# Optimization experiments

Hardware: AMD Instinct MI355X
Metric: run time of the kernel (lower is better)

## Reference

```python
import jax, jax.numpy as jnp
from jax import lax
import numpy as np

B, D, L = 32, 64, 4096
E = 8          # num_experts
K = 2          # top-k
OC = 32        # out_channels


def setup_inputs() -> dict:
    key = jax.random.key(0)
    ks = jax.random.split(key, 6)
    x = jax.random.normal(ks[0], (B, D, L), dtype=jnp.float32)
    # gating weight [D*5, E] (torch init is zeros; use small random for a meaningful reference)
    w_gate = jax.random.normal(ks[1], (D * 5, E), dtype=jnp.float32) * 0.02
    # Conv1d(D -> OC, kernel 3)
    conv1_w = jax.random.normal(ks[2], (OC, D, 3), dtype=jnp.float32) * (1.0 / np.sqrt(D * 3))
    conv1_b = jax.random.normal(ks[3], (OC,), dtype=jnp.float32) * 0.01
    # Conv1d(OC -> OC*E, kernel 1)
    conv2_w = jax.random.normal(ks[4], (OC * E, OC, 1), dtype=jnp.float32) * (1.0 / np.sqrt(OC))
    conv2_b = jax.random.normal(ks[5], (OC * E,), dtype=jnp.float32) * 0.01
    return {"x": x, "w_gate": w_gate, "conv1_w": conv1_w, "conv1_b": conv1_b,
            "conv2_w": conv2_w, "conv2_b": conv2_b}


def _gates(g_in, w_gate):
    # eval-mode noisy_top_k_gating: no noise, softmax -> top-(k+1) -> renormalize top-k -> scatter
    logits = jax.nn.softmax(g_in @ w_gate, axis=1)            # [B, E]
    top_v, top_i = lax.top_k(logits, min(K + 1, E))           # sorted descending
    vk = top_v[:, :K]
    ik = top_i[:, :K]
    gk = vk / (jnp.sum(vk, axis=1, keepdims=True) + 1e-6)
    gates = jnp.zeros_like(logits).at[jnp.arange(logits.shape[0])[:, None], ik].set(gk)
    return gates


def reference(x, w_gate, conv1_w, conv1_b, conv2_w, conv2_b):
    b, d, l = x.shape
    g_in = x[:, :, -6:-1].reshape(b, d * 5)                   # last-5-timestep gating features
    gates = _gates(g_in, w_gate)                              # [B, E]
    dn = ("NCH", "OIH", "NCH")
    h = lax.conv_general_dilated(x, conv1_w, (1,), "VALID", dimension_numbers=dn)
    h = jnp.tanh(h + conv1_b[None, :, None])                  # [B, OC, L-2]
    out = lax.conv_general_dilated(h, conv2_w, (1,), "VALID", dimension_numbers=dn)
    out = out + conv2_b[None, :, None]                        # [B, OC*E, L']
    lp = out.shape[-1]
    out = out.transpose(0, 2, 1).reshape(b, lp, OC, E)        # [B, L', OC, E]
    moe = jnp.einsum("blde,be->bld", out, gates)              # weighted combine
    return moe.transpose(0, 2, 1)                             # [B, OC, L']
```

## Files before the change

kernel.cpp:

```cpp
#include <hip/hip_runtime.h>
#include <math.h>

#define B_  32
#define D_  64
#define L_  4096
#define E_  8
#define OC_ 32
#define LP_ 4094

typedef __attribute__((ext_vector_type(8)))  short short8;
typedef __attribute__((ext_vector_type(16))) float float16;

static __device__ __forceinline__ unsigned cvtpk(float a, float b) {
    unsigned r;
    asm("v_cvt_pk_bf16_f32 %0, %1, %2" : "=v"(r) : "v"(a), "v"(b));
    return r;
}
static __device__ __forceinline__ float fast_tanh(float x) {
    float e = __expf(2.0f * x);
    return fmaf(-2.0f, __builtin_amdgcn_rcpf(e + 1.0f), 1.0f);
}

__global__ __launch_bounds__(256, 4)
void fused_all(const float* __restrict__ x,
               const float* __restrict__ w_gate,
               const float* __restrict__ c1w,
               const float* __restrict__ c1b,
               const float* __restrict__ c2w,
               const float* __restrict__ c2b,
               float* __restrict__ out)
{
    __shared__ __align__(16) unsigned short xT[132 * 64];
    __shared__ __align__(16) unsigned short aFl[12 * 64 * 8];
    __shared__ __align__(16) unsigned short a2L[2 * 64 * 8];
    __shared__ float gF[2];
    __shared__ int   gI[2];

    const int tid  = threadIdx.x;
    const int lane = tid & 63;
    const int wv   = tid >> 6;
    const int b    = blockIdx.x >> 5;
    const int l0   = (blockIdx.x & 31) << 7;
    const float* xb = x + (size_t)b * (D_ * L_);

    const int c2 = tid >> 3;
    const int jb = (tid & 7) << 2;
    const float* p0 = xb + (size_t)(2 * c2) * L_ + l0;
    const float* p1 = p0 + L_;
    float4 A0[4], A1[4];
    #pragma unroll
    for (int jq = 0; jq < 4; ++jq) {
        int j = jq * 32 + jb;
        A0[jq] = *(const float4*)(p0 + j);
        A1[jq] = *(const float4*)(p1 + j);
    }
    float hA0 = 0.f, hA1 = 0.f;
    const int haloc = tid >> 1, haloj = tid & 1;
    if (tid < 64) {
        int lg = l0 + 128 + haloj;
        if (lg < L_) {
            hA0 = xb[(size_t)(2 * haloc) * L_ + lg];
            hA1 = xb[(size_t)(2 * haloc + 1) * L_ + lg];
        }
    }

    const int w_oc = tid >> 3;
    const int w_c0 = (tid & 7) << 3;
    float wv24[24];
    {
        const float* wp = c1w + w_oc * 192 + w_c0 * 3;
        #pragma unroll
        for (int q = 0; q < 6; ++q)
            *(float4*)(wv24 + 4 * q) = *(const float4*)(wp + 4 * q);
    }

    if (wv == 0) {
        const int d = lane;
        float part[E_];
        #pragma unroll
        for (int e = 0; e < E_; ++e) part[e] = 0.f;
        #pragma unroll
        for (int t = 0; t < 5; ++t) {
            float xvt = xb[(size_t)d * L_ + (L_ - 6) + t];
            const float* wgp = w_gate + (d * 5 + t) * E_;
            float4 wa = *(const float4*)wgp;
            float4 wb = *(const float4*)(wgp + 4);
            part[0] = fmaf(xvt, wa.x, part[0]);
            part[1] = fmaf(xvt, wa.y, part[1]);
            part[2] = fmaf(xvt, wa.z, part[2]);
            part[3] = fmaf(xvt, wa.w, part[3]);
            part[4] = fmaf(xvt, wb.x, part[4]);
            part[5] = fmaf(xvt, wb.y, part[5]);
            part[6] = fmaf(xvt, wb.z, part[6]);
            part[7] = fmaf(xvt, wb.w, part[7]);
        }
        #pragma unroll
        for (int off = 1; off < 64; off <<= 1) {
            #pragma unroll
            for (int e = 0; e < E_; ++e)
                part[e] += __shfl_xor(part[e], off, 64);
        }
        float m = part[0];
        #pragma unroll
        for (int e = 1; e < E_; ++e) m = fmaxf(m, part[e]);
        float p[E_], s = 0.f;
        #pragma unroll
        for (int e = 0; e < E_; ++e) { p[e] = expf(part[e] - m); s += p[e]; }
        float inv = 1.f / s;
        #pragma unroll
        for (int e = 0; e < E_; ++e) p[e] *= inv;

        int i0 = 0;
        #pragma unroll
        for (int e = 1; e < E_; ++e) if (p[e] > p[i0]) i0 = e;
        int i1 = (i0 == 0) ? 1 : 0;
        #pragma unroll
        for (int e = 0; e < E_; ++e) {
            if (e == i0) continue;
            if (p[e] > p[i1]) i1 = e;
        }
        const float v0 = p[i0], v1 = p[i1];
        const float den = v0 + v1 + 1e-6f;
        const float g0 = v0 / den, g1 = v1 / den;

        const int cl0 = lane & 31;
        const int hi0 = lane >> 5;
        #pragma unroll
        for (int ks = 0; ks < 2; ++ks) {
            const float* q0 = c2w + (cl0 * E_ + i0) * OC_ + ks * 16 + hi0 * 8;
            const float* q1 = c2w + (cl0 * E_ + i1) * OC_ + ks * 16 + hi0 * 8;
            float4 u0a = *(const float4*)q0, u0b = *(const float4*)(q0 + 4);
            float4 u1a = *(const float4*)q1, u1b = *(const float4*)(q1 + 4);
            union { short8 s8; unsigned u[4]; } f;
            f.u[0] = cvtpk(fmaf(g0, u0a.x, g1 * u1a.x), fmaf(g0, u0a.y, g1 * u1a.y));
            f.u[1] = cvtpk(fmaf(g0, u0a.z, g1 * u1a.z), fmaf(g0, u0a.w, g1 * u1a.w));
            f.u[2] = cvtpk(fmaf(g0, u0b.x, g1 * u1b.x), fmaf(g0, u0b.y, g1 * u1b.y));
            f.u[3] = cvtpk(fmaf(g0, u0b.z, g1 * u1b.z), fmaf(g0, u0b.w, g1 * u1b.w));
            *(short8*)(a2L + (ks * 64 + lane) * 8) = f.s8;
        }
        if (lane == 0) {
            gF[0] = g0; gF[1] = g1;
            gI[0] = i0; gI[1] = i1;
        }
    }

    {
        const int ksoff = w_c0 >> 4;
        const int half  = (w_c0 >> 3) & 1;
        #pragma unroll
        for (int t = 0; t < 3; ++t) {
            union { short8 s8; unsigned u[4]; } w8;
            #pragma unroll
            for (int jj = 0; jj < 4; ++jj)
                w8.u[jj] = cvtpk(wv24[(2 * jj) * 3 + t], wv24[(2 * jj + 1) * 3 + t]);
            int base = ((t * 4 + ksoff) * 64 + half * 32 + w_oc) * 8;
            *(short8*)(aFl + base) = w8.s8;
        }
    }

    #pragma unroll
    for (int jq = 0; jq < 4; ++jq) {
        float e0[4] = {A0[jq].x, A0[jq].y, A0[jq].z, A0[jq].w};
        float e1[4] = {A1[jq].x, A1[jq].y, A1[jq].z, A1[jq].w};
        #pragma unroll
        for (int r = 0; r < 4; ++r) {
            int row = jq * 32 + jb + r;
            int off = (row * 128 + c2 * 4) ^ ((row & 7) << 4);
            *(unsigned*)((char*)xT + off) = cvtpk(e0[r], e1[r]);
        }
    }
    if (tid < 64) {
        int row = 128 + haloj;
        int off = (row * 128 + haloc * 4) ^ ((row & 7) << 4);
        *(unsigned*)((char*)xT + off) = cvtpk(hA0, hA1);
    }

    __syncthreads();

    const int cl = lane & 31;
    const int hi = lane >> 5;
    short8 a1[12];
    #pragma unroll
    for (int ks = 0; ks < 12; ++ks)
        a1[ks] = *(const short8*)(aFl + (ks * 64 + lane) * 8);
    short8 a2[2];
    a2[0] = *(const short8*)(a2L + (0 * 64 + lane) * 8);
    a2[1] = *(const short8*)(a2L + (1 * 64 + lane) * 8);
    const float g0 = gF[0], g1 = gF[1];
    const int   i0 = gI[0], i1 = gI[1];

    const int cb = wv * 32;
    float16 acc = (float16)0.0f;
    #pragma unroll
    for (int t = 0; t < 3; ++t) {
        int row = cb + cl + t;
        int rb  = row * 128;
        int swz = (row & 7) << 4;
        #pragma unroll
        for (int q = 0; q < 4; ++q) {
            int off = (rb + q * 32 + hi * 16) ^ swz;
            short8 bf = *(const short8*)((const char*)xT + off);
            acc = __builtin_amdgcn_mfma_f32_32x32x16_bf16(a1[t * 4 + q], bf, acc, 0, 0, 0);
        }
    }

    float th[16];
    #pragma unroll
    for (int r = 0; r < 16; ++r) {
        int row = (r & 3) + 8 * (r >> 2) + 4 * hi;
        th[r] = fast_tanh(acc[r] + c1b[row]);
    }

    unsigned x0a = hi ? cvtpk(th[0],  th[1])  : cvtpk(th[4],  th[5]);
    unsigned x0b = hi ? cvtpk(th[2],  th[3])  : cvtpk(th[6],  th[7]);
    unsigned x1a = hi ? cvtpk(th[8],  th[9])  : cvtpk(th[12], th[13]);
    unsigned x1b = hi ? cvtpk(th[10], th[11]) : cvtpk(th[14], th[15]);
    unsigned r0a = (unsigned)__shfl_xor((int)x0a, 32, 64);
    unsigned r0b = (unsigned)__shfl_xor((int)x0b, 32, 64);
    unsigned r1a = (unsigned)__shfl_xor((int)x1a, 32, 64);
    unsigned r1b = (unsigned)__shfl_xor((int)x1b, 32, 64);

    union U { short8 s8; unsigned u[4]; };
    U b0, b1;
    b0.u[0] = hi ? r0a : cvtpk(th[0], th[1]);
    b0.u[1] = hi ? r0b : cvtpk(th[2], th[3]);
    b0.u[2] = hi ? cvtpk(th[4], th[5]) : r0a;
    b0.u[3] = hi ? cvtpk(th[6], th[7]) : r0b;
    b1.u[0] = hi ? r1a : cvtpk(th[8], th[9]);
    b1.u[1] = hi ? r1b : cvtpk(th[10], th[11]);
    b1.u[2] = hi ? cvtpk(th[12], th[13]) : r1a;
    b1.u[3] = hi ? cvtpk(th[14], th[15]) : r1b;

    float16 acc2 = (float16)0.0f;
    acc2 = __builtin_amdgcn_mfma_f32_32x32x16_bf16(a2[0], b0.s8, acc2, 0, 0, 0);
    acc2 = __builtin_amdgcn_mfma_f32_32x32x16_bf16(a2[1], b1.s8, acc2, 0, 0, 0);

    int l = l0 + cb + cl;
    if (l < LP_) {
        float* ob = out + (size_t)b * (OC_ * (size_t)LP_) + l;
        #pragma unroll
        for (int r = 0; r < 16; ++r) {
            int row = (r & 3) + 8 * (r >> 2) + 4 * hi;
            float bb = fmaf(g0, c2b[row * E_ + i0], g1 * c2b[row * E_ + i1]);
            ob[(size_t)row * LP_] = acc2[r] + bb;
        }
    }
}

extern "C" void kernel_launch(void* const* d_in, const int* in_sizes, int n_in,
                              void* d_out, int out_size, void* d_ws, size_t ws_size,
                              hipStream_t stream)
{
    const float* x      = (const float*)d_in[0];
    const float* w_gate = (const float*)d_in[1];
    const float* c1w    = (const float*)d_in[2];
    const float* c1b    = (const float*)d_in[3];
    const float* c2w    = (const float*)d_in[4];
    const float* c2b    = (const float*)d_in[5];
    float* out = (float*)d_out;

    fused_all<<<B_ * 32, 256, 0, stream>>>(x, w_gate, c1w, c1b, c2w, c2b, out);
}
```

Baseline: 20.05 us.

## Enlarge per-block tile to 512 columns with 512 threads and two sub-tiles

Each block now covers 512 sequence positions using 512 threads: it loads two 256-column x tiles into separate LDS buffers and runs the conv/MoE tile compute twice. The aim is to amortize the per-block gating computation, weight staging and halo loads over more output, cutting redundant work across the 1024 blocks the old launch used. In exchange the grid shrinks to 256 blocks, about one per CU, with launch bounds of one block per SM. That lowers occupancy and latency hiding, and the two tiles are processed serially after a single sync.

```diff
diff --git a/kernel.cpp b/kernel.cpp
--- a/kernel.cpp
+++ b/kernel.cpp
@@ -21,7 +21,74 @@
     return fmaf(-2.0f, __builtin_amdgcn_rcpf(e + 1.0f), 1.0f);
 }
 
-__global__ __launch_bounds__(256, 4)
+static __device__ __forceinline__ void compute_tile(
+    const unsigned short* __restrict__ xbuf,
+    const short8* a1, const short8* a2,
+    const float* __restrict__ c1b,
+    const float* __restrict__ c2b,
+    int i0, int i1, float g0, float g1,
+    float* __restrict__ outb,
+    int l0, int wv, int cl, int hi)
+{
+    const int cb = wv * 32;
+    float16 acc = (float16)0.0f;
+    #pragma unroll
+    for (int t = 0; t < 3; ++t) {
+        int row = cb + cl + t;
+        int rb  = row * 128;
+        int swz = (row & 7) << 4;
+        #pragma unroll
+        for (int q = 0; q < 4; ++q) {
+            int off = (rb + q * 32 + hi * 16) ^ swz;
+            short8 bf = *(const short8*)((const char*)xbuf + off);
+            acc = __builtin_amdgcn_mfma_f32_32x32x16_bf16(a1[t * 4 + q], bf, acc, 0, 0, 0);
+        }
+    }
+
+    float th[16];
+    #pragma unroll
+    for (int r = 0; r < 16; ++r) {
+        int row = (r & 3) + 8 * (r >> 2) + 4 * hi;
+        th[r] = fast_tanh(acc[r] + c1b[row]);
+    }
+
+    unsigned x0a = hi ? cvtpk(th[0],  th[1])  : cvtpk(th[4],  th[5]);
+    unsigned x0b = hi ? cvtpk(th[2],  th[3])  : cvtpk(th[6],  th[7]);
+    unsigned x1a = hi ? cvtpk(th[8],  th[9])  : cvtpk(th[12], th[13]);
+    unsigned x1b = hi ? cvtpk(th[10], th[11]) : cvtpk(th[14], th[15]);
+    unsigned r0a = (unsigned)__shfl_xor((int)x0a, 32, 64);
+    unsigned r0b = (unsigned)__shfl_xor((int)x0b, 32, 64);
+    unsigned r1a = (unsigned)__shfl_xor((int)x1a, 32, 64);
+    unsigned r1b = (unsigned)__shfl_xor((int)x1b, 32, 64);
+
+    union U { short8 s8; unsigned u[4]; };
+    U b0, b1;
+    b0.u[0] = hi ? r0a : cvtpk(th[0], th[1]);
+    b0.u[1] = hi ? r0b : cvtpk(th[2], th[3]);
+    b0.u[2] = hi ? cvtpk(th[4], th[5]) : r0a;
+    b0.u[3] = hi ? cvtpk(th[6], th[7]) : r0b;
+    b1.u[0] = hi ? r1a : cvtpk(th[8], th[9]);
+    b1.u[1] = hi ? r1b : cvtpk(th[10], th[11]);
+    b1.u[2] = hi ? cvtpk(th[12], th[13]) : r1a;
+    b1.u[3] = hi ? cvtpk(th[14], th[15]) : r1b;
+
+    float16 acc2 = (float16)0.0f;
+    acc2 = __builtin_amdgcn_mfma_f32_32x32x16_bf16(a2[0], b0.s8, acc2, 0, 0, 0);
+    acc2 = __builtin_amdgcn_mfma_f32_32x32x16_bf16(a2[1], b1.s8, acc2, 0, 0, 0);
+
+    int l = l0 + cb + cl;
+    if (l < LP_) {
+        float* ob = outb + l;
+        #pragma unroll
+        for (int r = 0; r < 16; ++r) {
+            int row = (r & 3) + 8 * (r >> 2) + 4 * hi;
+            float bb = fmaf(g0, c2b[row * E_ + i0], g1 * c2b[row * E_ + i1]);
+            ob[(size_t)row * LP_] = acc2[r] + bb;
+        }
+    }
+}
+
+__global__ __launch_bounds__(512, 1)
 void fused_all(const float* __restrict__ x,
                const float* __restrict__ w_gate,
                const float* __restrict__ c1w,
@@ -30,7 +97,8 @@
                const float* __restrict__ c2b,
                float* __restrict__ out)
 {
-    __shared__ __align__(16) unsigned short xT[132 * 64];
+    __shared__ __align__(16) unsigned short xT0[260 * 64];
+    __shared__ __align__(16) unsigned short xT1[260 * 64];
     __shared__ __align__(16) unsigned short aFl[12 * 64 * 8];
     __shared__ __align__(16) unsigned short a2L[2 * 64 * 8];
     __shared__ float gF[2];
@@ -39,35 +107,42 @@
     const int tid  = threadIdx.x;
     const int lane = tid & 63;
     const int wv   = tid >> 6;
-    const int b    = blockIdx.x >> 5;
-    const int l0   = (blockIdx.x & 31) << 7;
+    const int b    = blockIdx.x >> 3;
+    const int S    = (blockIdx.x & 7) << 9;
     const float* xb = x + (size_t)b * (D_ * L_);
 
-    const int c2 = tid >> 3;
-    const int jb = (tid & 7) << 2;
-    const float* p0 = xb + (size_t)(2 * c2) * L_ + l0;
+    const int c2 = tid >> 4;
+    const int jb = (tid & 15) << 2;
+    const float* p0 = xb + (size_t)(2 * c2) * L_;
     const float* p1 = p0 + L_;
-    float4 A0[4], A1[4];
+    const int haloc = tid >> 1;
+    const int haloj = tid & 1;
+
+    float4 A0[4], A1[4], B0[4], B1[4];
     #pragma unroll
     for (int jq = 0; jq < 4; ++jq) {
-        int j = jq * 32 + jb;
+        int j = S + jq * 64 + jb;
         A0[jq] = *(const float4*)(p0 + j);
         A1[jq] = *(const float4*)(p1 + j);
-    }
-    float hA0 = 0.f, hA1 = 0.f;
-    const int haloc = tid >> 1, haloj = tid & 1;
+        B0[jq] = *(const float4*)(p0 + 256 + j);
+        B1[jq] = *(const float4*)(p1 + 256 + j);
+    }
+    float hA0 = 0.f, hA1 = 0.f, hB0 = 0.f, hB1 = 0.f;
     if (tid < 64) {
-        int lg = l0 + 128 + haloj;
-        if (lg < L_) {
-            hA0 = xb[(size_t)(2 * haloc) * L_ + lg];
-            hA1 = xb[(size_t)(2 * haloc + 1) * L_ + lg];
-        }
-    }
-
-    const int w_oc = tid >> 3;
-    const int w_c0 = (tid & 7) << 3;
+        int lgA = S + 256 + haloj;
+        hA0 = xb[(size_t)(2 * haloc) * L_ + lgA];
+        hA1 = xb[(size_t)(2 * haloc + 1) * L_ + lgA];
+        int lgB = S + 512 + haloj;
+        if (lgB > L_ - 1) lgB = L_ - 1;
+        hB0 = xb[(size_t)(2 * haloc) * L_ + lgB];
+        hB1 = xb[(size_t)(2 * haloc + 1) * L_ + lgB];
+    }
+
+    const int tid2 = tid - 256;
+    const int w_oc = tid2 >> 3;
+    const int w_c0 = (tid2 & 7) << 3;
     float wv24[24];
-    {
+    if (tid >= 256) {
         const float* wp = c1w + w_oc * 192 + w_c0 * 3;
         #pragma unroll
         for (int q = 0; q < 6; ++q)
@@ -144,7 +219,7 @@
         }
     }
 
-    {
+    if (tid >= 256) {
         const int ksoff = w_c0 >> 4;
         const int half  = (w_c0 >> 3) & 1;
         #pragma unroll
@@ -162,17 +237,21 @@
     for (int jq = 0; jq < 4; ++jq) {
         float e0[4] = {A0[jq].x, A0[jq].y, A0[jq].z, A0[jq].w};
         float e1[4] = {A1[jq].x, A1[jq].y, A1[jq].z, A1[jq].w};
+        float f0[4] = {B0[jq].x, B0[jq].y, B0[jq].z, B0[jq].w};
+        float f1[4] = {B1[jq].x, B1[jq].y, B1[jq].z, B1[jq].w};
         #pragma unroll
         for (int r = 0; r < 4; ++r) {
-            int row = jq * 32 + jb + r;
+            int row = jq * 64 + jb + r;
             int off = (row * 128 + c2 * 4) ^ ((row & 7) << 4);
-            *(unsigned*)((char*)xT + off) = cvtpk(e0[r], e1[r]);
+            *(unsigned*)((char*)xT0 + off) = cvtpk(e0[r], e1[r]);
+            *(unsigned*)((char*)xT1 + off) = cvtpk(f0[r], f1[r]);
         }
     }
     if (tid < 64) {
-        int row = 128 + haloj;
+        int row = 256 + haloj;
         int off = (row * 128 + haloc * 4) ^ ((row & 7) << 4);
-        *(unsigned*)((char*)xT + off) = cvtpk(hA0, hA1);
+        *(unsigned*)((char*)xT0 + off) = cvtpk(hA0, hA1);
+        *(unsigned*)((char*)xT1 + off) = cvtpk(hB0, hB1);
     }
 
     __syncthreads();
@@ -189,62 +268,10 @@
     const float g0 = gF[0], g1 = gF[1];
     const int   i0 = gI[0], i1 = gI[1];
 
-    const int cb = wv * 32;
-    float16 acc = (float16)0.0f;
-    #pragma unroll
-    for (int t = 0; t < 3; ++t) {
-        int row = cb + cl + t;
-        int rb  = row * 128;
-        int swz = (row & 7) << 4;
-        #pragma unroll
-        for (int q = 0; q < 4; ++q) {
-            int off = (rb + q * 32 + hi * 16) ^ swz;
-            short8 bf = *(const short8*)((const char*)xT + off);
-            acc = __builtin_amdgcn_mfma_f32_32x32x16_bf16(a1[t * 4 + q], bf, acc, 0, 0, 0);
-        }
-    }
-
-    float th[16];
-    #pragma unroll
-    for (int r = 0; r < 16; ++r) {
-        int row = (r & 3) + 8 * (r >> 2) + 4 * hi;
-        th[r] = fast_tanh(acc[r] + c1b[row]);
-    }
-
-    unsigned x0a = hi ? cvtpk(th[0],  th[1])  : cvtpk(th[4],  th[5]);
-    unsigned x0b = hi ? cvtpk(th[2],  th[3])  : cvtpk(th[6],  th[7]);
-    unsigned x1a = hi ? cvtpk(th[8],  th[9])  : cvtpk(th[12], th[13]);
-    unsigned x1b = hi ? cvtpk(th[10], th[11]) : cvtpk(th[14], th[15]);
-    unsigned r0a = (unsigned)__shfl_xor((int)x0a, 32, 64);
-    unsigned r0b = (unsigned)__shfl_xor((int)x0b, 32, 64);
-    unsigned r1a = (unsigned)__shfl_xor((int)x1a, 32, 64);
-    unsigned r1b = (unsigned)__shfl_xor((int)x1b, 32, 64);
-
-    union U { short8 s8; unsigned u[4]; };
-    U b0, b1;
-    b0.u[0] = hi ? r0a : cvtpk(th[0], th[1]);
-    b0.u[1] = hi ? r0b : cvtpk(th[2], th[3]);
-    b0.u[2] = hi ? cvtpk(th[4], th[5]) : r0a;
-    b0.u[3] = hi ? cvtpk(th[6], th[7]) : r0b;
-    b1.u[0] = hi ? r1a : cvtpk(th[8], th[9]);
-    b1.u[1] = hi ? r1b : cvtpk(th[10], th[11]);
-    b1.u[2] = hi ? cvtpk(th[12], th[13]) : r1a;
-    b1.u[3] = hi ? cvtpk(th[14], th[15]) : r1b;
-
-    float16 acc2 = (float16)0.0f;
-    acc2 = __builtin_amdgcn_mfma_f32_32x32x16_bf16(a2[0], b0.s8, acc2, 0, 0, 0);
-    acc2 = __builtin_amdgcn_mfma_f32_32x32x16_bf16(a2[1], b1.s8, acc2, 0, 0, 0);
-
-    int l = l0 + cb + cl;
-    if (l < LP_) {
-        float* ob = out + (size_t)b * (OC_ * (size_t)LP_) + l;
-        #pragma unroll
-        for (int r = 0; r < 16; ++r) {
-            int row = (r & 3) + 8 * (r >> 2) + 4 * hi;
-            float bb = fmaf(g0, c2b[row * E_ + i0], g1 * c2b[row * E_ + i1]);
-            ob[(size_t)row * LP_] = acc2[r] + bb;
-        }
-    }
+    float* outb = out + (size_t)b * (OC_ * (size_t)LP_);
+
+    compute_tile(xT0, a1, a2, c1b, c2b, i0, i1, g0, g1, outb, S,       wv, cl, hi);
+    compute_tile(xT1, a1, a2, c1b, c2b, i0, i1, g0, g1, outb, S + 256, wv, cl, hi);
 }
 
 extern "C" void kernel_launch(void* const* d_in, const int* in_sizes, int n_in,
@@ -259,5 +286,5 @@
     const float* c2b    = (const float*)d_in[5];
     float* out = (float*)d_out;
 
-    fused_all<<<B_ * 32, 256, 0, stream>>>(x, w_gate, c1w, c1b, c2w, c2b, out);
-}
+    fused_all<<<B_ * 8, 512, 0, stream>>>(x, w_gate, c1w, c1b, c2w, c2b, out);
+}
```

New measurement: 19.46 us. 1.03x faster.
